# Performance work log

Measured on AMD Instinct MI355X. Metric: run time of the kernel, lower is better.

## Reference

```python
import jax, jax.numpy as jnp
import numpy as np

# ---- module hyperparameters (from init_kwargs) ----
K = 8            # kernel_size
DIL = 1          # dilation
ZERO_LAG = True  # include_zero_lag
C_IN = 32
C_OUT = 32
HID = 64
EPS = 1e-5       # BatchNorm eps

# position_vec[i] = 10000 ** (2*(i//2)/in_channels)
_POS_VEC = jnp.asarray(np.array([10000.0 ** (2.0 * (i // 2) / C_IN) for i in range(C_IN)], dtype=np.float32))


def setup_inputs() -> dict:
    key = jax.random.key(0)
    ks = jax.random.split(key, 10)
    bs, L = 4, 2048
    # strictly increasing event times per sequence
    times = jnp.cumsum(jax.random.uniform(ks[0], (bs, L), dtype=jnp.float32) * 0.1, axis=1)
    features = jax.random.normal(ks[1], (bs, L, C_IN), dtype=jnp.float32)
    # trailing padding: random valid lengths in [L//2, L]
    lengths = jax.random.randint(ks[2], (bs,), L // 2, L + 1)
    non_pad_mask = jnp.arange(L)[None, :] < lengths[:, None]
    s = lambda fan: 1.0 / np.sqrt(fan)
    W1 = jax.random.normal(ks[3], (C_IN, HID), dtype=jnp.float32) * s(C_IN)
    b1 = jnp.zeros((HID,), jnp.float32)
    W2 = jax.random.normal(ks[4], (HID, C_IN * C_OUT), dtype=jnp.float32) * s(HID)
    b2 = jnp.zeros((C_IN * C_OUT,), jnp.float32)
    W_skip = jax.random.normal(ks[5], (C_IN, C_OUT), dtype=jnp.float32) * s(C_IN)
    b_skip = jnp.zeros((C_OUT,), jnp.float32)
    gamma = jnp.ones((C_OUT,), jnp.float32)
    beta = jnp.zeros((C_OUT,), jnp.float32)
    return {"times": times, "features": features, "non_pad_mask": non_pad_mask,
            "W1": W1, "b1": b1, "W2": W2, "b2": b2,
            "W_skip": W_skip, "b_skip": b_skip, "gamma": gamma, "beta": beta}


def _temporal_enc(dt):
    # dt: (bs,K,L) -> (bs,K,L,C_IN); even dims sin, odd dims cos
    r = dt[..., None] / _POS_VEC
    even = (jnp.arange(C_IN) % 2) == 0
    return jnp.where(even, jnp.sin(r), jnp.cos(r))


def reference(times, features, non_pad_mask, W1, b1, W2, b2, W_skip, b_skip, gamma, beta):
    bs, L = times.shape
    # --- windowed gather (equivalent to conv1d with identity kernel + trim) ---
    pad = (K - 1) * DIL if ZERO_LAG else K * DIL
    idx = jnp.arange(L)[None, :] - pad + jnp.arange(K)[:, None] * DIL   # (K,L)
    valid = idx >= 0
    idx_c = jnp.clip(idx, 0, L - 1)
    t_g = times[:, idx_c]                                               # (bs,K,L)
    m_g = non_pad_mask[:, idx_c] & valid[None]                          # (bs,K,L)
    dt_mask = m_g & non_pad_mask[:, None, :]                            # (bs,K,L)
    delta_times = jnp.where(dt_mask, times[:, None, :] - t_g, 0.0)      # (bs,K,L)
    feat_g = jnp.where(dt_mask[..., None], features[:, idx_c, :], 0.0)  # (bs,K,L,C_IN)
    # --- per-tap kernel MLP ---
    te = _temporal_enc(delta_times)                                     # (bs,K,L,C_IN)
    h = jax.nn.relu(te @ W1 + b1)                                       # (bs,K,L,HID)
    kv = (h @ W2 + b2).reshape(bs, K, L, C_IN, C_OUT)                   # (bs,K,L,C_IN,C_OUT)
    kv = jnp.where(dt_mask[..., None, None], kv, 0.0)
    # --- multiply-reduce over taps and input channels ---
    out = jnp.einsum('bktc,bktco->bto', feat_g, kv)                     # (bs,L,C_OUT)
    # --- skip connection (1x1 conv) ---
    out = out + features @ W_skip + b_skip
    # --- BatchNorm1d over channels, batch statistics (training mode) ---
    mean = out.mean(axis=(0, 1))
    var = out.var(axis=(0, 1))
    out = gamma * (out - mean) / jnp.sqrt(var + EPS) + beta
    return out
```

## Files before the change

kernel.cpp:

```cpp
#include <hip/hip_runtime.h>

#define L 2048
#define BS 4
#define CIN 32
#define COUT 32
#define HIDN 64
#define KK 8
#define TB 8
#define EPSV 1e-5f
#define QSTR (HIDN*CIN + 8)

typedef _Float16 f16;
typedef _Float16 f16x2 __attribute__((ext_vector_type(2)));
typedef _Float16 f16x8 __attribute__((ext_vector_type(8)));
typedef __fp16   h16x2 __attribute__((ext_vector_type(2)));
typedef float    f32x2 __attribute__((ext_vector_type(2)));
typedef float    f32x4 __attribute__((ext_vector_type(4)));

__global__ __launch_bounds__(64) void prep(const float* __restrict__ W2,
                                           const float* __restrict__ W1,
                                           f16* __restrict__ w2h,
                                           f16* __restrict__ w1p,
                                           float* __restrict__ sums) {
    const int f    = blockIdx.x;
    const int lane = threadIdx.x;
    if (f == 128) {
        #pragma unroll
        for (int i2 = 0; i2 < 16; i2++) {
            w1p[lane*32 + i2*2 + 0] = (f16)W1[(2*i2 + 0)*HIDN + lane];
            w1p[lane*32 + i2*2 + 1] = (f16)W1[(2*i2 + 1)*HIDN + lane];
        }
        return;
    }
    if (f == 0) {
        #pragma unroll
        for (int j = 0; j < 8; j++) sums[j*64 + lane] = 0.f;
    }
    const int kb = f >> 1, nt = f & 1;
    const int m = lane & 15, qd = lane >> 4;
    #pragma unroll
    for (int j = 0; j < 8; j++)
        w2h[(f*64 + lane)*8 + j] = (f16)W2[(kb*32 + qd*8 + j)*32 + nt*16 + m];
}

__global__ __launch_bounds__(256, 4) void cc_main(
    const float* __restrict__ times,
    const float* __restrict__ features,
    const int*   __restrict__ mask,
    const float* __restrict__ b1,
    const float* __restrict__ b2,
    const float* __restrict__ Wsk,
    const float* __restrict__ bsk,
    const f16*   __restrict__ w2h,
    const f16*   __restrict__ w1p,
    float* __restrict__ out,
    float* __restrict__ sums)
{
    __shared__ __align__(16) char s_pool[TB * QSTR * 2];
    f16   (*s_Q )[QSTR]     = (f16  (*)[QSTR])    s_pool;
    f16   (*s_te)[KK][CIN]  = (f16  (*)[KK][CIN]) s_pool;
    float (*s_f )[KK][CIN]  = (float(*)[KK][CIN])(s_pool + 4096);
    __shared__ float s_F [TB][CIN];
    __shared__ float s_ft[TB][CIN];
    __shared__ float s_part[4][TB][COUT];

    const int tid = threadIdx.x;
    const int tl  = tid >> 5;
    const int x   = tid & 31;
    const int bt  = blockIdx.x * TB + tl;
    const int b   = bt >> 11;
    const int t   = bt & (L - 1);

    union UH { f16x8 v8[4]; f16x2 d2[16]; } wa, wb;
    #pragma unroll
    for (int i = 0; i < 4; i++) {
        wa.v8[i] = ((const f16x8*)(w1p + x*32))[i];
        wb.v8[i] = ((const f16x8*)(w1p + (x + 32)*32))[i];
    }
    const float b1a = b1[x], b1b = b1[x + 32];

    const float t_cur = times[b*L + t];
    const int   np_t  = mask[b*L + t];
    float tv[KK], fr[KK];
    int   mv[KK];
    #pragma unroll
    for (int k = 0; k < KK; k++) {
        const int idx  = t - (KK - 1) + k;
        const int idxc = idx > 0 ? idx : 0;
        tv[k] = times[b*L + idxc];
        mv[k] = mask[b*L + idxc];
        fr[k] = features[(b*L + idxc)*CIN + x];
    }
    const float inv_pos = exp2f(-(float)(x >> 1) * (13.2877123795f / 16.0f));
    float Fx = 0.f;
    #pragma unroll
    for (int k = 0; k < KK; k++) {
        const int dm  = (t - (KK - 1) + k >= 0) && np_t && mv[k];
        const float r = (t_cur - tv[k]) * inv_pos;
        s_te[tl][k][x] = (f16)((x & 1) ? __cosf(r) : __sinf(r));
        const float fv = dm ? fr[k] : 0.f;
        s_f[tl][k][x] = fv;
        Fx += fv;
    }
    s_F [tl][x] = Fx;
    s_ft[tl][x] = features[(b*L + t)*CIN + x];
    __syncthreads();

    f32x2 q0[16], q1[16];
    #pragma unroll
    for (int c = 0; c < 16; c++) { q0[c] = (f32x2){0.f,0.f}; q1[c] = (f32x2){0.f,0.f}; }

    #pragma unroll
    for (int k = 0; k < KK; k++) {
        union UT { f16x8 v8[4]; f16x2 d2[16]; } te;
        union UF { f32x4 v4[8]; f32x2 d2[16]; } ff;
        #pragma unroll
        for (int i = 0; i < 4; i++) te.v8[i] = ((const f16x8*)&s_te[tl][k][0])[i];
        #pragma unroll
        for (int i = 0; i < 8; i++) ff.v4[i] = ((const f32x4*)&s_f[tl][k][0])[i];

        float a0 = 0.f, a1 = 0.f, a2 = 0.f, a3 = 0.f;
        float c0 = 0.f, c1 = 0.f, c2 = 0.f, c3 = 0.f;
        #pragma unroll
        for (int g = 0; g < 4; g++) {
            a0 = __builtin_amdgcn_fdot2(te.d2[g*4+0], wa.d2[g*4+0], a0, false);
            a1 = __builtin_amdgcn_fdot2(te.d2[g*4+1], wa.d2[g*4+1], a1, false);
            a2 = __builtin_amdgcn_fdot2(te.d2[g*4+2], wa.d2[g*4+2], a2, false);
            a3 = __builtin_amdgcn_fdot2(te.d2[g*4+3], wa.d2[g*4+3], a3, false);
            c0 = __builtin_amdgcn_fdot2(te.d2[g*4+0], wb.d2[g*4+0], c0, false);
            c1 = __builtin_amdgcn_fdot2(te.d2[g*4+1], wb.d2[g*4+1], c1, false);
            c2 = __builtin_amdgcn_fdot2(te.d2[g*4+2], wb.d2[g*4+2], c2, false);
            c3 = __builtin_amdgcn_fdot2(te.d2[g*4+3], wb.d2[g*4+3], c3, false);
        }
        const float ha = fmaxf(((a0 + a1) + (a2 + a3)) + b1a, 0.f);
        const float hb = fmaxf(((c0 + c1) + (c2 + c3)) + b1b, 0.f);
        const f32x2 h2a = {ha, ha}, h2b = {hb, hb};
        #pragma unroll
        for (int c = 0; c < 16; c++) {
            q0[c] = h2a * ff.d2[c] + q0[c];
            q1[c] = h2b * ff.d2[c] + q1[c];
        }
    }
    __syncthreads();

    const int sw = x & 7;
    #pragma unroll
    for (int cj = 0; cj < 4; cj++) {
        union { f16x8 v8; h16x2 v2[4]; } p0, p1;
        #pragma unroll
        for (int j = 0; j < 4; j++) {
            p0.v2[j] = __builtin_amdgcn_cvt_pkrtz(q0[cj*4 + j][0], q0[cj*4 + j][1]);
            p1.v2[j] = __builtin_amdgcn_cvt_pkrtz(q1[cj*4 + j][0], q1[cj*4 + j][1]);
        }
        const int ch0 = ((x*4 + cj) ^ sw);
        const int ch1 = (((x + 32)*4 + cj) ^ sw);
        *(f16x8*)&s_Q[tl][ch0*8] = p0.v8;
        *(f16x8*)&s_Q[tl][ch1*8] = p1.v8;
    }

    float ex = bsk[x];
    #pragma unroll
    for (int c = 0; c < CIN; c++) ex = fmaf(s_ft[tl][c], Wsk[c*COUT + x], ex);
    #pragma unroll
    for (int c = 0; c < CIN; c++) ex = fmaf(s_F [tl][c], b2 [c*COUT + x], ex);
    __syncthreads();

    {
        const int wv   = tid >> 6;
        const int lane = tid & 63;
        const int m    = lane & 15, qd = lane >> 4;
        const int row  = m & 7;
        f32x4 C0 = {0.f,0.f,0.f,0.f}, C1 = {0.f,0.f,0.f,0.f};
        #pragma unroll 4
        for (int kb = wv*16; kb < wv*16 + 16; kb++) {
            const int ch = ((kb*4 + qd) ^ (kb & 7));
            const f16x8 a   = *(const f16x8*)&s_Q[row][ch*8];
            const f16x8 bf0 = ((const f16x8*)w2h)[(kb*2 + 0)*64 + lane];
            const f16x8 bf1 = ((const f16x8*)w2h)[(kb*2 + 1)*64 + lane];
            C0 = __builtin_amdgcn_mfma_f32_16x16x32_f16(a, bf0, C0, 0, 0, 0);
            C1 = __builtin_amdgcn_mfma_f32_16x16x32_f16(a, bf1, C1, 0, 0, 0);
        }
        if (qd < 2) {
            #pragma unroll
            for (int r = 0; r < 4; r++) {
                s_part[wv][qd*4 + r][m]      = C0[r];
                s_part[wv][qd*4 + r][16 + m] = C1[r];
            }
        }
    }
    __syncthreads();

    float val = ex;
    #pragma unroll
    for (int w = 0; w < 4; w++) val += s_part[w][tl][x];
    out[(b*L + t)*COUT + x] = val;

    s_F [tl][x] = val;
    s_ft[tl][x] = val * val;
    __syncthreads();
    if (tid < 32) {
        float s1 = 0.f, s2 = 0.f;
        #pragma unroll
        for (int j = 0; j < TB; j++) { s1 += s_F[j][x]; s2 += s_ft[j][x]; }
        float* shard = sums + (blockIdx.x & 7) * 64;
        atomicAdd(&shard[x],      s1);
        atomicAdd(&shard[32 + x], s2);
    }
}

__global__ __launch_bounds__(256) void cc_norm(
    float4* __restrict__ out, const float* __restrict__ sums,
    const float* __restrict__ gamma, const float* __restrict__ beta)
{
    const int i  = blockIdx.x * 256 + threadIdx.x;
    const int o0 = (i & 7) * 4;
    const float n = (float)(BS * L);
    float4 v = out[i], r;
    float* vp = &v.x; float* rp = &r.x;
    #pragma unroll
    for (int j = 0; j < 4; j++) {
        const int o = o0 + j;
        float s1 = 0.f, s2 = 0.f;
        #pragma unroll
        for (int s = 0; s < 8; s++) { s1 += sums[s*64 + o]; s2 += sums[s*64 + 32 + o]; }
        const float mean = s1 / n;
        const float var  = s2 / n - mean * mean;
        rp[j] = gamma[o] * (vp[j] - mean) * rsqrtf(var + EPSV) + beta[o];
    }
    out[i] = r;
}

extern "C" void kernel_launch(void* const* d_in, const int* in_sizes, int n_in,
                              void* d_out, int out_size, void* d_ws, size_t ws_size,
                              hipStream_t stream) {
    const float* times    = (const float*)d_in[0];
    const float* features = (const float*)d_in[1];
    const int*   mask     = (const int*)  d_in[2];
    const float* W1       = (const float*)d_in[3];
    const float* b1       = (const float*)d_in[4];
    const float* W2       = (const float*)d_in[5];
    const float* b2       = (const float*)d_in[6];
    const float* Wsk      = (const float*)d_in[7];
    const float* bsk      = (const float*)d_in[8];
    const float* gamma    = (const float*)d_in[9];
    const float* beta     = (const float*)d_in[10];
    float* out  = (float*)d_out;
    float* sums = (float*)d_ws;
    f16*   w2h  = (f16*)((char*)d_ws + 4096);
    f16*   w1p  = (f16*)((char*)d_ws + 4096 + 131072);

    prep<<<129, 64, 0, stream>>>(W2, W1, w2h, w1p, sums);
    cc_main<<<(BS*L)/TB, 256, 0, stream>>>(times, features, mask, b1,
                                           b2, Wsk, bsk, w2h, w1p, out, sums);
    cc_norm<<<(BS*L*COUT)/(4*256), 256, 0, stream>>>((float4*)out, sums, gamma, beta);
}
```

Measured before the change: 95.52 us.

## Fuse weight prep into main kernel with flag sync and 16-row MFMA tiles

Removes the separate prep kernel. The first 128 blocks of the main kernel now convert W2 to fp16 and signal completion through an agent-scope counter, and every block spins on that counter before its MFMA stage. W1 is converted inline per block. The tile grows from 8 to 16 timesteps per 512-thread block, so each 16x16 MFMA tile uses all its rows instead of duplicating 8, and s_part now reuses the shared pool. The aim is to drop a kernel launch and wasted MFMA work. The cost is spin-wait synchronisation that relies on the prep blocks being resident, and a flag and counter reset that can race with blocks from the same launch on repeated calls.

Result: slower. 110.2 us (+15.4%).

```diff
diff --git a/kernel.cpp b/kernel.cpp
--- a/kernel.cpp
+++ b/kernel.cpp
@@ -6,9 +6,12 @@
 #define COUT 32
 #define HIDN 64
 #define KK 8
-#define TB 8
+#define TB 16
+#define NBLK ((BS*L)/TB)
 #define EPSV 1e-5f
 #define QSTR (HIDN*CIN + 8)
+#define NPREP 128
+#define MAGIC 0x51CAFE17
 
 typedef _Float16 f16;
 typedef _Float16 f16x2 __attribute__((ext_vector_type(2)));
@@ -17,65 +20,72 @@
 typedef float    f32x2 __attribute__((ext_vector_type(2)));
 typedef float    f32x4 __attribute__((ext_vector_type(4)));
 
-__global__ __launch_bounds__(64) void prep(const float* __restrict__ W2,
-                                           const float* __restrict__ W1,
-                                           f16* __restrict__ w2h,
-                                           f16* __restrict__ w1p,
-                                           float* __restrict__ sums) {
-    const int f    = blockIdx.x;
-    const int lane = threadIdx.x;
-    if (f == 128) {
-        #pragma unroll
-        for (int i2 = 0; i2 < 16; i2++) {
-            w1p[lane*32 + i2*2 + 0] = (f16)W1[(2*i2 + 0)*HIDN + lane];
-            w1p[lane*32 + i2*2 + 1] = (f16)W1[(2*i2 + 1)*HIDN + lane];
-        }
-        return;
-    }
-    if (f == 0) {
-        #pragma unroll
-        for (int j = 0; j < 8; j++) sums[j*64 + lane] = 0.f;
-    }
-    const int kb = f >> 1, nt = f & 1;
-    const int m = lane & 15, qd = lane >> 4;
-    #pragma unroll
-    for (int j = 0; j < 8; j++)
-        w2h[(f*64 + lane)*8 + j] = (f16)W2[(kb*32 + qd*8 + j)*32 + nt*16 + m];
-}
-
-__global__ __launch_bounds__(256, 4) void cc_main(
+__global__ __launch_bounds__(512, 4) void cc_main(
     const float* __restrict__ times,
     const float* __restrict__ features,
     const int*   __restrict__ mask,
+    const float* __restrict__ W1,
     const float* __restrict__ b1,
+    const float* __restrict__ W2,
     const float* __restrict__ b2,
     const float* __restrict__ Wsk,
     const float* __restrict__ bsk,
-    const f16*   __restrict__ w2h,
-    const f16*   __restrict__ w1p,
     float* __restrict__ out,
-    float* __restrict__ sums)
+    float* __restrict__ sums,
+    int*   __restrict__ init_flag,
+    int*   __restrict__ prep_ctr,
+    f16*   __restrict__ w2h)
 {
     __shared__ __align__(16) char s_pool[TB * QSTR * 2];
-    f16   (*s_Q )[QSTR]     = (f16  (*)[QSTR])    s_pool;
-    f16   (*s_te)[KK][CIN]  = (f16  (*)[KK][CIN]) s_pool;
-    float (*s_f )[KK][CIN]  = (float(*)[KK][CIN])(s_pool + 4096);
+    f16   (*s_Q )[QSTR]      = (f16  (*)[QSTR])    s_pool;
+    f16   (*s_te)[KK][CIN]   = (f16  (*)[KK][CIN]) s_pool;
+    float (*s_f )[KK][CIN]   = (float(*)[KK][CIN])(s_pool + 8192);
+    float (*s_part)[TB][COUT]= (float(*)[TB][COUT])s_pool;
     __shared__ float s_F [TB][CIN];
     __shared__ float s_ft[TB][CIN];
-    __shared__ float s_part[4][TB][COUT];
 
     const int tid = threadIdx.x;
     const int tl  = tid >> 5;
     const int x   = tid & 31;
-    const int bt  = blockIdx.x * TB + tl;
+    const int bid = blockIdx.x;
+    const int bt  = bid * TB + tl;
     const int b   = bt >> 11;
     const int t   = bt & (L - 1);
 
-    union UH { f16x8 v8[4]; f16x2 d2[16]; } wa, wb;
-    #pragma unroll
-    for (int i = 0; i < 4; i++) {
-        wa.v8[i] = ((const f16x8*)(w1p + x*32))[i];
-        wb.v8[i] = ((const f16x8*)(w1p + (x + 32)*32))[i];
+    if (bid == 0) {
+        sums[tid] = 0.f;
+        if (tid == 0) *prep_ctr = 0;
+        __threadfence();
+        __syncthreads();
+        if (tid == 0)
+            __hip_atomic_store(init_flag, MAGIC, __ATOMIC_RELEASE, __HIP_MEMORY_SCOPE_AGENT);
+    }
+
+    if (bid < NPREP) {
+        if (tid < 64) {
+            const int kb = bid >> 1, nt = bid & 1;
+            const int mm = tid & 15, qq = tid >> 4;
+            const float* src = W2 + (kb*32 + qq*8)*32 + nt*16 + mm;
+            union { f16x8 v8; h16x2 v2[4]; } p;
+            #pragma unroll
+            for (int jj = 0; jj < 4; jj++)
+                p.v2[jj] = __builtin_amdgcn_cvt_pkrtz(src[(2*jj)*32], src[(2*jj+1)*32]);
+            *(f16x8*)&w2h[(bid*64 + tid)*8] = p.v8;
+        }
+        if (tid == 0) {
+            while (__hip_atomic_load(init_flag, __ATOMIC_ACQUIRE, __HIP_MEMORY_SCOPE_AGENT) != MAGIC)
+                __builtin_amdgcn_s_sleep(1);
+            __hip_atomic_fetch_add(prep_ctr, 1, __ATOMIC_RELEASE, __HIP_MEMORY_SCOPE_AGENT);
+        }
+    }
+
+    union UH { f16x8 v8[4]; f16x2 d2[16]; h16x2 p2[16]; } wa, wb;
+    #pragma unroll
+    for (int i2 = 0; i2 < 16; i2++) {
+        wa.p2[i2] = __builtin_amdgcn_cvt_pkrtz(W1[(2*i2)*HIDN + x],
+                                               W1[(2*i2+1)*HIDN + x]);
+        wb.p2[i2] = __builtin_amdgcn_cvt_pkrtz(W1[(2*i2)*HIDN + x + 32],
+                                               W1[(2*i2+1)*HIDN + x + 32]);
     }
     const float b1a = b1[x], b1b = b1[x + 32];
 
@@ -163,36 +173,39 @@
     for (int c = 0; c < CIN; c++) ex = fmaf(s_ft[tl][c], Wsk[c*COUT + x], ex);
     #pragma unroll
     for (int c = 0; c < CIN; c++) ex = fmaf(s_F [tl][c], b2 [c*COUT + x], ex);
+
+    if (tid == 0) {
+        while (__hip_atomic_load(prep_ctr, __ATOMIC_ACQUIRE, __HIP_MEMORY_SCOPE_AGENT) != NPREP)
+            __builtin_amdgcn_s_sleep(2);
+    }
     __syncthreads();
 
     {
         const int wv   = tid >> 6;
         const int lane = tid & 63;
         const int m    = lane & 15, qd = lane >> 4;
-        const int row  = m & 7;
         f32x4 C0 = {0.f,0.f,0.f,0.f}, C1 = {0.f,0.f,0.f,0.f};
-        #pragma unroll 4
-        for (int kb = wv*16; kb < wv*16 + 16; kb++) {
+        #pragma unroll
+        for (int kb = wv*8; kb < wv*8 + 8; kb++) {
             const int ch = ((kb*4 + qd) ^ (kb & 7));
-            const f16x8 a   = *(const f16x8*)&s_Q[row][ch*8];
+            const f16x8 a   = *(const f16x8*)&s_Q[m][ch*8];
             const f16x8 bf0 = ((const f16x8*)w2h)[(kb*2 + 0)*64 + lane];
             const f16x8 bf1 = ((const f16x8*)w2h)[(kb*2 + 1)*64 + lane];
             C0 = __builtin_amdgcn_mfma_f32_16x16x32_f16(a, bf0, C0, 0, 0, 0);
             C1 = __builtin_amdgcn_mfma_f32_16x16x32_f16(a, bf1, C1, 0, 0, 0);
         }
-        if (qd < 2) {
-            #pragma unroll
-            for (int r = 0; r < 4; r++) {
-                s_part[wv][qd*4 + r][m]      = C0[r];
-                s_part[wv][qd*4 + r][16 + m] = C1[r];
-            }
+        __syncthreads();
+        #pragma unroll
+        for (int r = 0; r < 4; r++) {
+            s_part[wv][qd*4 + r][m]      = C0[r];
+            s_part[wv][qd*4 + r][16 + m] = C1[r];
         }
     }
     __syncthreads();
 
     float val = ex;
     #pragma unroll
-    for (int w = 0; w < 4; w++) val += s_part[w][tl][x];
+    for (int w = 0; w < 8; w++) val += s_part[w][tl][x];
     out[(b*L + t)*COUT + x] = val;
 
     s_F [tl][x] = val;
@@ -202,7 +215,7 @@
         float s1 = 0.f, s2 = 0.f;
         #pragma unroll
         for (int j = 0; j < TB; j++) { s1 += s_F[j][x]; s2 += s_ft[j][x]; }
-        float* shard = sums + (blockIdx.x & 7) * 64;
+        float* shard = sums + (bid & 7) * 64;
         atomicAdd(&shard[x],      s1);
         atomicAdd(&shard[32 + x], s2);
     }
@@ -245,12 +258,13 @@
     const float* gamma    = (const float*)d_in[9];
     const float* beta     = (const float*)d_in[10];
     float* out  = (float*)d_out;
-    float* sums = (float*)d_ws;
-    f16*   w2h  = (f16*)((char*)d_ws + 4096);
-    f16*   w1p  = (f16*)((char*)d_ws + 4096 + 131072);
-
-    prep<<<129, 64, 0, stream>>>(W2, W1, w2h, w1p, sums);
-    cc_main<<<(BS*L)/TB, 256, 0, stream>>>(times, features, mask, b1,
-                                           b2, Wsk, bsk, w2h, w1p, out, sums);
+
+    float* sums      = (float*)d_ws;
+    int*   init_flag = (int*)((char*)d_ws + 2048);
+    int*   prep_ctr  = (int*)((char*)d_ws + 2052);
+    f16*   w2h       = (f16*)((char*)d_ws + 4096);
+
+    cc_main<<<NBLK, 512, 0, stream>>>(times, features, mask, W1, b1, W2, b2,
+                                      Wsk, bsk, out, sums, init_flag, prep_ctr, w2h);
     cc_norm<<<(BS*L*COUT)/(4*256), 256, 0, stream>>>((float4*)out, sums, gamma, beta);
 }
```
